# Kernel tuning notes

Measured on AMD Instinct MI355X. Metric: run time of the kernel, lower is better.

## Reference

```python
import jax, jax.numpy as jnp
import numpy as np
import math

N, S, D, H, L, F = 4, 2048, 512, 8, 4, 200
HD = D // H
EPS = 1e-5


def _pos_encoding(seq_len, d_model, dtype):
    pos = jnp.arange(seq_len, dtype=jnp.float32)[:, None]            # [S,1]
    div = jnp.exp(jnp.arange(0, d_model, 2, dtype=jnp.float32) * (-math.log(10000.0) / d_model))
    ang = pos * div                                                   # [S,D/2]
    pe = jnp.stack([jnp.sin(ang), jnp.cos(ang)], axis=-1).reshape(seq_len, d_model)
    return pe.astype(dtype)


def _layernorm(x, w, b):
    mu = jnp.mean(x, axis=-1, keepdims=True)
    var = jnp.mean(jnp.square(x - mu), axis=-1, keepdims=True)
    return (x - mu) * jax.lax.rsqrt(var + EPS) * w + b


def setup_inputs() -> dict:
    key = jax.random.key(0)
    ks = jax.random.split(key, 8)
    std = 0.02
    inp = {
        "features": jax.random.normal(ks[0], (N, S, D), dtype=jnp.float32),
        # attention projections, stored as [L, in, out] (math-equivalent to torch x @ W.T + b)
        "Wq": jax.random.normal(ks[1], (L, D, D), dtype=jnp.float32) * std,
        "bq": jnp.zeros((L, D), dtype=jnp.float32),
        "Wk": jax.random.normal(ks[2], (L, D, D), dtype=jnp.float32) * std,
        "bk": jnp.zeros((L, D), dtype=jnp.float32),
        "Wv": jax.random.normal(ks[3], (L, D, D), dtype=jnp.float32) * std,
        "bv": jnp.zeros((L, D), dtype=jnp.float32),
        "Wo": jax.random.normal(ks[4], (L, D, D), dtype=jnp.float32) * std,
        "bo": jnp.zeros((L, D), dtype=jnp.float32),
        # FFN
        "W1": jax.random.normal(ks[5], (L, D, F), dtype=jnp.float32) * std,
        "b1": jnp.zeros((L, F), dtype=jnp.float32),
        "W2": jax.random.normal(ks[6], (L, F, D), dtype=jnp.float32) * std,
        "b2": jnp.zeros((L, D), dtype=jnp.float32),
        # layernorms
        "ln1_w": jnp.ones((L, D), dtype=jnp.float32),
        "ln1_b": jnp.zeros((L, D), dtype=jnp.float32),
        "ln2_w": jnp.ones((L, D), dtype=jnp.float32),
        "ln2_b": jnp.zeros((L, D), dtype=jnp.float32),
    }
    return inp


def _encoder(features, Wq, bq, Wk, bk, Wv, bv, Wo, bo, W1, b1, W2, b2,
             ln1_w, ln1_b, ln2_w, ln2_b):
    n, s, d = features.shape
    x = features + _pos_encoding(s, d, features.dtype)[None]  # PositionalEncoding (dropout=identity in eval)
    scale = 1.0 / math.sqrt(HD)
    for l in range(L):
        # MultiHeadAttention: manual QK^T -> softmax -> AV
        q = (x @ Wq[l] + bq[l]).reshape(n, s, H, HD)
        k = (x @ Wk[l] + bk[l]).reshape(n, s, H, HD)
        v = (x @ Wv[l] + bv[l]).reshape(n, s, H, HD)
        attn = jnp.einsum("nshd,nthd->nhst", q, k) * scale          # [N,H,S,S]
        score = jax.nn.softmax(attn, axis=-1)
        y = jnp.einsum("nhst,nthd->nshd", score, v).reshape(n, s, d)
        attn_out = y @ Wo[l] + bo[l]
        x = _layernorm(x + attn_out, ln1_w[l], ln1_b[l])
        # FFN: linear2(relu(linear1(x)))
        ff = jax.nn.relu(x @ W1[l] + b1[l]) @ W2[l] + b2[l]
        x = _layernorm(x + ff, ln2_w[l], ln2_b[l])
    return x


def reference(features, Wq, bq, Wk, bk, Wv, bv, Wo, bo, W1, b1, W2, b2,
              ln1_w, ln1_b, ln2_w, ln2_b):
    return _encoder(features, Wq, bq, Wk, bk, Wv, bv, Wo, bo, W1, b1, W2, b2,
                    ln1_w, ln1_b, ln2_w, ln2_b)
```

## Files before the change

### kernel.cpp

```cpp
#include <hip/hip_runtime.h>
#include <hip/hip_bf16.h>
#include <cstdint>


typedef __bf16 bf16;
typedef __bf16 bf16x8 __attribute__((ext_vector_type(8)));
typedef __bf16 bf16x4 __attribute__((ext_vector_type(4)));
typedef float f32x4 __attribute__((ext_vector_type(4)));

#define MFMA16(a, b, c) __builtin_amdgcn_mfma_f32_16x16x32_bf16((a), (b), (c), 0, 0, 0)

static constexpr int NB   = 4;
static constexpr int SQ   = 2048;
static constexpr int DM   = 512;
static constexpr int NH   = 8;
static constexpr int HD   = 64;
static constexpr int NL   = 4;
static constexpr int FF   = 200;
static constexpr int FFP  = 256;
static constexpr int MTOK = NB * SQ;

__device__ __forceinline__ float fast_exp2(float x) {
#if __has_builtin(__builtin_amdgcn_exp2f)
    return __builtin_amdgcn_exp2f(x);
#else
    return exp2f(x);
#endif
}

__device__ __forceinline__ void gld16(bf16* l, const bf16* g) {
    __builtin_amdgcn_global_load_lds(
        (const __attribute__((address_space(1))) void*)g,
        (__attribute__((address_space(3))) void*)l, 16, 0, 0);
}

__device__ __forceinline__ void drain_and_barrier() {
    asm volatile("s_waitcnt vmcnt(0) lgkmcnt(0)" ::: "memory");
    __builtin_amdgcn_s_barrier();
}

__global__ __launch_bounds__(256) void convw_kernel(
    const float* __restrict__ Wq, const float* __restrict__ Wk,
    const float* __restrict__ Wv, const float* __restrict__ Wo,
    const float* __restrict__ W1, const float* __restrict__ W2,
    bf16* __restrict__ wqkvt, bf16* __restrict__ wot,
    bf16* __restrict__ w1t, bf16* __restrict__ w2t)
{
    __shared__ float tile[32][33];
    const int z = blockIdx.z, l = z / 6, which = z % 6;
    const float* src; bf16* dst; int K, Nsrc, Npad, Kpad;
    switch (which) {
        case 0: src = Wq + (size_t)l*DM*DM; dst = wqkvt + (size_t)(l*3+0)*DM*DM; K=DM; Nsrc=DM; Npad=DM; Kpad=DM; break;
        case 1: src = Wk + (size_t)l*DM*DM; dst = wqkvt + (size_t)(l*3+1)*DM*DM; K=DM; Nsrc=DM; Npad=DM; Kpad=DM; break;
        case 2: src = Wv + (size_t)l*DM*DM; dst = wqkvt + (size_t)(l*3+2)*DM*DM; K=DM; Nsrc=DM; Npad=DM; Kpad=DM; break;
        case 3: src = Wo + (size_t)l*DM*DM; dst = wot   + (size_t)l*DM*DM;       K=DM; Nsrc=DM; Npad=DM; Kpad=DM; break;
        case 4: src = W1 + (size_t)l*DM*FF; dst = w1t   + (size_t)l*FFP*DM;      K=DM; Nsrc=FF; Npad=FFP; Kpad=DM; break;
        default:src = W2 + (size_t)l*FF*DM; dst = w2t   + (size_t)l*DM*FFP;      K=FF; Nsrc=DM; Npad=DM; Kpad=FFP; break;
    }
    const int k0 = blockIdx.x * 32, n0 = blockIdx.y * 32;
    if (k0 >= Kpad || n0 >= Npad) return;
    const int tr = threadIdx.x >> 3, tc = (threadIdx.x & 7) * 4;
    for (int c = 0; c < 4; c++) {
        int sr = k0 + tr, sc = n0 + tc + c;
        tile[tr][tc + c] = (sr < K && sc < Nsrc) ? src[(size_t)sr * Nsrc + sc] : 0.f;
    }
    __syncthreads();
    const int dr = n0 + tr;
    if (dr < Npad) {
        for (int c = 0; c < 4; c++) {
            int dc = k0 + tc + c;
            if (dc < Kpad) dst[(size_t)dr * Kpad + dc] = (bf16)tile[tc + c][tr];
        }
    }
}

__global__ __launch_bounds__(256) void posenc_kernel(
    const float* __restrict__ f, float* __restrict__ x, bf16* __restrict__ xb)
{
    const int t = blockIdx.x * 256 + threadIdx.x;
    const int d2 = t & 255, row = t >> 8, s = row & (SQ - 1);
    const float kfac = -0.03597789207803197f;
    float dv = __expf((float)d2 * kfac);
    float ang = (float)s * dv;
    float pe0 = sinf(ang), pe1 = cosf(ang);
    const size_t base = (size_t)row * DM + d2 * 2;
    float2 fv = *(const float2*)(f + base);
    float o0 = fv.x + pe0, o1 = fv.y + pe1;
    *(float2*)(x + base) = make_float2(o0, o1);
    union { bf16 h[2]; unsigned int u; } pk;
    pk.h[0] = (bf16)o0; pk.h[1] = (bf16)o1;
    *(unsigned int*)(xb + base) = pk.u;
}

__device__ __forceinline__ void gemm128_core(
    const bf16* __restrict__ A, const bf16* __restrict__ Wt, int K,
    int m0, int n0, bf16* As, bf16* Bs, f32x4 (&acc)[4][4])
{
    const int tid = threadIdx.x;
    const int w = tid >> 6, lane = tid & 63;
    const int l15 = lane & 15, quad = lane >> 4;
    const int srow = w * 16 + (lane >> 2);
    const int scol = (lane & 3) * 8;
    const bf16* Ag = A  + (size_t)(m0 + srow) * K + scol;
    const bf16* Bg = Wt + (size_t)(n0 + srow) * K + scol;
    const int wm = (w >> 1) * 64, wn = (w & 1) * 64;

    auto stage = [&](int buf, int k0) {
        bf16* AsW = As + buf * 4096 + w * 512;
        bf16* BsW = Bs + buf * 4096 + w * 512;
        gld16(AsW,        Ag + k0);
        gld16(AsW + 2048, Ag + (size_t)64 * K + k0);
        gld16(BsW,        Bg + k0);
        gld16(BsW + 2048, Bg + (size_t)64 * K + k0);
    };

    stage(0, 0);
    drain_and_barrier();

    const int nsteps = K >> 5;
    int buf = 0;
    for (int t = 0; t < nsteps; ++t) {
        if (t + 1 < nsteps) stage(buf ^ 1, (t + 1) << 5);
        const bf16* AsR = As + buf * 4096;
        const bf16* BsR = Bs + buf * 4096;
        bf16x8 af[4], bfr[4];
        #pragma unroll
        for (int i = 0; i < 4; i++)
            af[i] = *(const bf16x8*)&AsR[(wm + i * 16 + l15) * 32 + quad * 8];
        #pragma unroll
        for (int j = 0; j < 4; j++)
            bfr[j] = *(const bf16x8*)&BsR[(wn + j * 16 + l15) * 32 + quad * 8];
        #pragma unroll
        for (int i = 0; i < 4; i++)
            #pragma unroll
            for (int j = 0; j < 4; j++)
                acc[i][j] = MFMA16(af[i], bfr[j], acc[i][j]);
        drain_and_barrier();
        buf ^= 1;
    }
}

__global__ __launch_bounds__(256, 4) void gemm64_kernel(
    const bf16* __restrict__ A, const bf16* __restrict__ Wt,
    const float* __restrict__ bias, int nbias,
    float* __restrict__ outf, bf16* __restrict__ outb,
    int K, int Nc, int mode)
{
    __shared__ alignas(16) bf16 As[2 * 128 * 32];
    __shared__ alignas(16) bf16 Bs[2 * 64 * 32];
    const int m0 = blockIdx.x * 128, n0 = blockIdx.y * 64;
    const int tid = threadIdx.x;
    const int w = tid >> 6, lane = tid & 63;
    const int l15 = lane & 15, quad = lane >> 4;
    const int srow = w * 16 + (lane >> 2);
    const int scol = (lane & 3) * 8;
    const bf16* Ag = A  + (size_t)(m0 + srow) * K + scol;
    const bf16* Bg = Wt + (size_t)(n0 + srow) * K + scol;
    const int wm = (w >> 1) * 64, wn = (w & 1) * 32;
    f32x4 acc[4][2] = {};

    auto stage = [&](int buf, int k0) {
        bf16* AsW = As + buf * 4096 + w * 512;
        bf16* BsW = Bs + buf * 2048 + w * 512;
        gld16(AsW,        Ag + k0);
        gld16(AsW + 2048, Ag + (size_t)64 * K + k0);
        gld16(BsW,        Bg + k0);
    };

    stage(0, 0);
    drain_and_barrier();

    const int nsteps = K >> 5;
    int buf = 0;
    for (int t = 0; t < nsteps; ++t) {
        if (t + 1 < nsteps) stage(buf ^ 1, (t + 1) << 5);
        const bf16* AsR = As + buf * 4096;
        const bf16* BsR = Bs + buf * 2048;
        bf16x8 af[4], bfr[2];
        #pragma unroll
        for (int i = 0; i < 4; i++)
            af[i] = *(const bf16x8*)&AsR[(wm + i * 16 + l15) * 32 + quad * 8];
        #pragma unroll
        for (int j = 0; j < 2; j++)
            bfr[j] = *(const bf16x8*)&BsR[(wn + j * 16 + l15) * 32 + quad * 8];
        #pragma unroll
        for (int i = 0; i < 4; i++)
            #pragma unroll
            for (int j = 0; j < 2; j++)
                acc[i][j] = MFMA16(af[i], bfr[j], acc[i][j]);
        drain_and_barrier();
        buf ^= 1;
    }

    #pragma unroll
    for (int j = 0; j < 2; j++) {
        const int col = n0 + wn + j * 16 + l15;
        const float bv = (col < nbias) ? bias[col] : 0.f;
        #pragma unroll
        for (int i = 0; i < 4; i++) {
            const int rbase = m0 + wm + i * 16 + quad * 4;
            #pragma unroll
            for (int r = 0; r < 4; r++) {
                float v = acc[i][j][r] + bv;
                const int row = rbase + r;
                const size_t idx = (size_t)row * Nc + col;
                if (mode == 0)      outf[idx] = v;
                else if (mode == 1) outb[idx] = (bf16)v;
                else                outb[idx] = (bf16)fmaxf(v, 0.f);
            }
        }
    }
}

__global__ __launch_bounds__(256, 4) void gemm_wo_kernel(
    const bf16* __restrict__ o0, const bf16* __restrict__ o1,
    const float* __restrict__ lpart,
    const bf16* __restrict__ Wt, const float* __restrict__ bias,
    float* __restrict__ outf)
{
    __shared__ alignas(16) bf16 As[2 * 128 * 32];
    __shared__ alignas(16) bf16 Bs[2 * 64 * 32];
    const int m0 = blockIdx.x * 128, n0 = blockIdx.y * 64;
    const int tid = threadIdx.x;
    const int w = tid >> 6, lane = tid & 63;
    const int l15 = lane & 15, quad = lane >> 4;
    const int srow = w * 16 + (lane >> 2);
    const int scol = (lane & 3) * 8;
    const int row0 = m0 + srow, row1 = row0 + 64;
    const bf16* Bg = Wt + (size_t)(n0 + srow) * DM + scol;
    const int wm = (w >> 1) * 64, wn = (w & 1) * 32;

    const int b0 = (((row0 >> 11) * 8) << 11) | (row0 & (SQ - 1));
    const int b1 = (((row1 >> 11) * 8) << 11) | (row1 & (SQ - 1));
    float rl0[8], rl1[8];
    #pragma unroll
    for (int h = 0; h < 8; h++) {
        rl0[h] = 1.f / (lpart[b0 + (h << 11)] + lpart[65536 + b0 + (h << 11)]);
        rl1[h] = 1.f / (lpart[b1 + (h << 11)] + lpart[65536 + b1 + (h << 11)]);
    }

    const bf16* A0g  = o0 + (size_t)row0 * DM + scol;
    const bf16* A0g2 = o0 + (size_t)row1 * DM + scol;
    const bf16* A1g  = o1 + (size_t)row0 * DM + scol;
    const bf16* A1g2 = o1 + (size_t)row1 * DM + scol;
    f32x4 acc[4][2] = {};

    auto combineStore = [&](int buf, int h, bf16x8 a0, bf16x8 c0, bf16x8 a1, bf16x8 c1) {
        bf16x8 s0, s1;
        #pragma unroll
        for (int i = 0; i < 8; i++) {
            s0[i] = (bf16)(((float)a0[i] + (float)c0[i]) * rl0[h]);
            s1[i] = (bf16)(((float)a1[i] + (float)c1[i]) * rl1[h]);
        }
        bf16* d = As + buf * 4096 + w * 512 + lane * 8;
        *(bf16x8*)d          = s0;
        *(bf16x8*)(d + 2048) = s1;
    };

    {
        bf16x8 a0 = *(const bf16x8*)(A0g);
        bf16x8 c0 = *(const bf16x8*)(A1g);
        bf16x8 a1 = *(const bf16x8*)(A0g2);
        bf16x8 c1 = *(const bf16x8*)(A1g2);
        gld16(Bs + w * 512, Bg);
        combineStore(0, 0, a0, c0, a1, c1);
        drain_and_barrier();
    }

    int buf = 0;
    for (int t = 0; t < 16; ++t) {
        const bool pre = (t + 1 < 16);
        bf16x8 na0, nc0, na1, nc1;
        if (pre) {
            const int k1 = (t + 1) * 32;
            na0 = *(const bf16x8*)(A0g  + k1);
            nc0 = *(const bf16x8*)(A1g  + k1);
            na1 = *(const bf16x8*)(A0g2 + k1);
            nc1 = *(const bf16x8*)(A1g2 + k1);
            gld16(Bs + (buf ^ 1) * 2048 + w * 512, Bg + k1);
        }

        const bf16* AsR = As + buf * 4096;
        const bf16* BsR = Bs + buf * 2048;
        bf16x8 af[4], bfr[2];
        #pragma unroll
        for (int i = 0; i < 4; i++)
            af[i] = *(const bf16x8*)&AsR[(wm + i * 16 + l15) * 32 + quad * 8];
        #pragma unroll
        for (int j = 0; j < 2; j++)
            bfr[j] = *(const bf16x8*)&BsR[(wn + j * 16 + l15) * 32 + quad * 8];
        #pragma unroll
        for (int i = 0; i < 4; i++)
            #pragma unroll
            for (int j = 0; j < 2; j++)
                acc[i][j] = MFMA16(af[i], bfr[j], acc[i][j]);

        if (pre) combineStore(buf ^ 1, (t + 1) >> 1, na0, nc0, na1, nc1);
        drain_and_barrier();
        buf ^= 1;
    }

    #pragma unroll
    for (int j = 0; j < 2; j++) {
        const int col = n0 + wn + j * 16 + l15;
        const float bv = bias[col];
        #pragma unroll
        for (int i = 0; i < 4; i++) {
            const int rbase = m0 + wm + i * 16 + quad * 4;
            #pragma unroll
            for (int r = 0; r < 4; r++)
                outf[(size_t)(rbase + r) * DM + col] = acc[i][j][r] + bv;
        }
    }
}

__global__ __launch_bounds__(256, 4) void gemm128_qkv_kernel(
    const bf16* __restrict__ xb, const bf16* __restrict__ Wt,
    const float* __restrict__ bq, const float* __restrict__ bk,
    const float* __restrict__ bv,
    bf16* __restrict__ qb, bf16* __restrict__ kb, bf16* __restrict__ vtb)
{
    __shared__ alignas(16) bf16 As[2 * 128 * 32];
    __shared__ alignas(16) bf16 Bs[2 * 128 * 32];
    const int m0 = blockIdx.x * 128, n0 = blockIdx.y * 128;
    f32x4 acc[4][4] = {};
    gemm128_core(xb, Wt, DM, m0, n0, As, Bs, acc);

    const int lane = threadIdx.x & 63;
    const int l15 = lane & 15, quad = lane >> 4;
    const int w = threadIdx.x >> 6;
    const int wm = (w >> 1) * 64, wn = (w & 1) * 64;
    const int which = n0 >> 9;
    const float* bias = (which == 0) ? bq : (which == 1) ? bk : bv;
    const float scale = (which == 0) ? 0.18033688f : 1.f;
    #pragma unroll
    for (int j = 0; j < 4; j++) {
        const int c = (n0 & 511) + wn + j * 16 + l15;
        const float bvv = bias[c];
        #pragma unroll
        for (int i = 0; i < 4; i++) {
            const int rbase = m0 + wm + i * 16 + quad * 4;
            if (which == 2) {
                union { bf16 h[4]; uint2 u2; } pk;
                #pragma unroll
                for (int r = 0; r < 4; r++)
                    pk.h[r] = (bf16)(acc[i][j][r] + bvv);
                const int n = rbase >> 11, s = rbase & (SQ - 1);
                const int h = c >> 6, hd = c & 63;
                *(uint2*)&vtb[((size_t)(((n << 3) | h) << 6 | hd) << 11) | s] = pk.u2;
            } else {
                #pragma unroll
                for (int r = 0; r < 4; r++) {
                    float v = (acc[i][j][r] + bvv) * scale;
                    const int row = rbase + r;
                    if (which == 0) qb[(size_t)row * DM + c] = (bf16)v;
                    else            kb[(size_t)row * DM + c] = (bf16)v;
                }
            }
        }
    }
}

__global__ __launch_bounds__(256, 2) void attn_kernel(
    const bf16* __restrict__ qb, const bf16* __restrict__ kb,
    const bf16* __restrict__ vtb,
    bf16* __restrict__ opart0, bf16* __restrict__ opart1,
    float* __restrict__ lpart)
{
    __shared__ alignas(16) bf16 Kt[2][64][72];
    __shared__ alignas(16) bf16 Vt[2 * 64 * 68];
    const int tid = threadIdx.x;
    const int w = tid >> 6, lane = tid & 63;
    const int l15 = lane & 15, quad = lane >> 4;
    const int id = blockIdx.x;
    const int kvhalf = id & 1;
    const int nh = (id >> 1) & 31;
    const int qblk = id >> 6;
    const int n = nh >> 3, h = nh & 7;
    const int q0 = qblk * 256 + w * 64;
    const int kvbase = kvhalf * (SQ / 2);
    const bf16* qbase = qb + (size_t)n * SQ * DM + h * HD;
    const bf16* kbase = kb + (size_t)n * SQ * DM + h * HD;
    const bf16* vbase = vtb + (size_t)nh * HD * SQ;

    bf16x8 qf[4][2];
    #pragma unroll
    for (int mi = 0; mi < 4; mi++)
        #pragma unroll
        for (int hh = 0; hh < 2; hh++)
            qf[mi][hh] = *(const bf16x8*)(qbase + (size_t)(q0 + mi*16 + l15) * DM + hh*32 + quad*8);

    bf16x8 ones8;
    #pragma unroll
    for (int i = 0; i < 8; i++) ones8[i] = (bf16)1.0f;

    f32x4 o[4][4] = {};
    f32x4 lacc[4] = {};

    const int srow = tid >> 2, seg = (tid & 3) * 16;
    const bf16* krow = kbase + (size_t)(kvbase + srow) * DM + seg;
    const bf16* vrow = vbase + (size_t)srow * SQ + kvbase + seg;

    auto storeV = [&](int buf, bf16x8 a, bf16x8 b) {
        bf16* d = &Vt[(buf * 64 + srow) * 68 + seg];
        bf16x4 p0, p1, p2, p3;
        #pragma unroll
        for (int i = 0; i < 4; i++) { p0[i]=a[i]; p1[i]=a[i+4]; p2[i]=b[i]; p3[i]=b[i+4]; }
        *(bf16x4*)(d)      = p0;
        *(bf16x4*)(d + 4)  = p1;
        *(bf16x4*)(d + 8)  = p2;
        *(bf16x4*)(d + 12) = p3;
    };

    {
        bf16x8 k0 = *(const bf16x8*)(krow);
        bf16x8 k1 = *(const bf16x8*)(krow + 8);
        bf16x8 v0 = *(const bf16x8*)(vrow);
        bf16x8 v1 = *(const bf16x8*)(vrow + 8);
        *(bf16x8*)&Kt[0][srow][seg]     = k0;
        *(bf16x8*)&Kt[0][srow][seg + 8] = k1;
        storeV(0, v0, v1);
    }

    const int NT = SQ / 128;
    for (int jt = 0; jt < NT; jt++) {
        const int buf = jt & 1;
        __syncthreads();
        const bool pre = (jt + 1 < NT);
        bf16x8 k0, k1, v0, v1;
        if (pre) {
            const bf16* kp = krow + (size_t)(jt + 1) * 64 * DM;
            const bf16* vp = vrow + (jt + 1) * 64;
            k0 = *(const bf16x8*)(kp);
            k1 = *(const bf16x8*)(kp + 8);
            v0 = *(const bf16x8*)(vp);
            v1 = *(const bf16x8*)(vp + 8);
        }

        #pragma unroll
        for (int sp = 0; sp < 2; sp++) {
            bf16x8 kfA0 = *(const bf16x8*)&Kt[buf][sp*32 + l15][quad*8];
            bf16x8 kfA1 = *(const bf16x8*)&Kt[buf][sp*32 + l15][32 + quad*8];
            bf16x8 kfB0 = *(const bf16x8*)&Kt[buf][sp*32 + 16 + l15][quad*8];
            bf16x8 kfB1 = *(const bf16x8*)&Kt[buf][sp*32 + 16 + l15][32 + quad*8];
            bf16x8 pf[4];
            #pragma unroll
            for (int mi = 0; mi < 4; mi++) {
                f32x4 sa = {}, sb = {};
                sa = MFMA16(kfA0, qf[mi][0], sa);
                sa = MFMA16(kfA1, qf[mi][1], sa);
                sb = MFMA16(kfB0, qf[mi][0], sb);
                sb = MFMA16(kfB1, qf[mi][1], sb);
                bf16x8 p;
                #pragma unroll
                for (int r = 0; r < 4; r++) {
                    p[r]     = (bf16)fast_exp2(sa[r]);
                    p[r + 4] = (bf16)fast_exp2(sb[r]);
                }
                pf[mi] = p;
                lacc[mi] = MFMA16(p, ones8, lacc[mi]);
            }
            #pragma unroll
            for (int d4 = 0; d4 < 4; d4++) {
                const bf16* vp2 = &Vt[(buf*64 + d4*16 + l15) * 68 + sp*32 + quad*4];
                bf16x4 vlo = *(const bf16x4*)(vp2);
                bf16x4 vhi = *(const bf16x4*)(vp2 + 16);
                bf16x8 vf;
                #pragma unroll
                for (int i = 0; i < 4; i++) { vf[i] = vlo[i]; vf[i+4] = vhi[i]; }
                #pragma unroll
                for (int mi = 0; mi < 4; mi++)
                    o[mi][d4] = MFMA16(pf[mi], vf, o[mi][d4]);
            }
        }

        if (pre) {
            *(bf16x8*)&Kt[buf^1][srow][seg]     = k0;
            *(bf16x8*)&Kt[buf^1][srow][seg + 8] = k1;
            storeV(buf^1, v0, v1);
        }
    }

    if (l15 == 0) {
        const int base = (kvhalf << 16) + (nh << 11) + q0 + quad * 4;
        #pragma unroll
        for (int mi = 0; mi < 4; mi++) {
            float4 v4 = make_float4(lacc[mi][0], lacc[mi][1], lacc[mi][2], lacc[mi][3]);
            *(float4*)&lpart[base + mi * 16] = v4;
        }
    }

    bf16* op = kvhalf ? opart1 : opart0;
    #pragma unroll
    for (int mi = 0; mi < 4; mi++) {
        #pragma unroll
        for (int d4 = 0; d4 < 4; d4++) {
            const int col = h * HD + d4 * 16 + l15;
            #pragma unroll
            for (int r = 0; r < 4; r++) {
                const int row = n * SQ + q0 + mi*16 + quad*4 + r;
                op[(size_t)row * DM + col] = (bf16)o[mi][d4][r];
            }
        }
    }
}

__global__ __launch_bounds__(256) void ln_kernel(
    const float* __restrict__ res, const float* __restrict__ add,
    const float* __restrict__ g, const float* __restrict__ beta,
    float* __restrict__ outf, bf16* __restrict__ outb)
{
    const int w = threadIdx.x >> 6, lane = threadIdx.x & 63;
    const size_t row = (size_t)blockIdx.x * 4 + w;
    const float4* rp = (const float4*)(res + row * DM);
    const float4* ap = (const float4*)(add + row * DM);
    float4 v[2];
    float s = 0.f, s2 = 0.f;
    #pragma unroll
    for (int i = 0; i < 2; i++) {
        const int idx = i * 64 + lane;
        float4 a = rp[idx], c = ap[idx];
        float x0 = a.x + c.x, x1 = a.y + c.y, x2 = a.z + c.z, x3 = a.w + c.w;
        v[i] = make_float4(x0, x1, x2, x3);
        s  += x0 + x1 + x2 + x3;
        s2 += x0*x0 + x1*x1 + x2*x2 + x3*x3;
    }
    for (int m = 1; m < 64; m <<= 1) {
        s  += __shfl_xor(s,  m, 64);
        s2 += __shfl_xor(s2, m, 64);
    }
    const float mean = s * (1.f / DM);
    const float var  = s2 * (1.f / DM) - mean * mean;
    const float rstd = rsqrtf(var + 1e-5f);
    #pragma unroll
    for (int i = 0; i < 2; i++) {
        const int idx = i * 64 + lane;
        float4 gw = ((const float4*)g)[idx], bw = ((const float4*)beta)[idx];
        float o0 = (v[i].x - mean) * rstd * gw.x + bw.x;
        float o1 = (v[i].y - mean) * rstd * gw.y + bw.y;
        float o2 = (v[i].z - mean) * rstd * gw.z + bw.z;
        float o3 = (v[i].w - mean) * rstd * gw.w + bw.w;
        ((float4*)(outf + row * DM))[idx] = make_float4(o0, o1, o2, o3);
        union { bf16 h[4]; uint2 u; } pk;
        pk.h[0] = (bf16)o0; pk.h[1] = (bf16)o1; pk.h[2] = (bf16)o2; pk.h[3] = (bf16)o3;
        *(uint2*)(outb + row * DM + idx * 4) = pk.u;
    }
}

extern "C" void kernel_launch(void* const* d_in, const int* in_sizes, int n_in,
                              void* d_out, int out_size, void* d_ws, size_t ws_size,
                              hipStream_t stream)
{
    const float* features = (const float*)d_in[0];
    const float* Wq  = (const float*)d_in[1];
    const float* bq  = (const float*)d_in[2];
    const float* Wk  = (const float*)d_in[3];
    const float* bk  = (const float*)d_in[4];
    const float* Wv  = (const float*)d_in[5];
    const float* bv  = (const float*)d_in[6];
    const float* Wo  = (const float*)d_in[7];
    const float* bo  = (const float*)d_in[8];
    const float* W1  = (const float*)d_in[9];
    const float* b1  = (const float*)d_in[10];
    const float* W2  = (const float*)d_in[11];
    const float* b2  = (const float*)d_in[12];
    const float* ln1w = (const float*)d_in[13];
    const float* ln1b = (const float*)d_in[14];
    const float* ln2w = (const float*)d_in[15];
    const float* ln2b = (const float*)d_in[16];
    float* outp = (float*)d_out;

    char* p = (char*)d_ws;
    size_t off = 0;
    auto alloc = [&](size_t bytes) { void* r = p + off; off = (off + bytes + 255) & ~(size_t)255; return r; };
    const size_t tokD = (size_t)MTOK * DM;
    float* x     = (float*)alloc(tokD * 4);
    float* tmp   = (float*)alloc(tokD * 4);
    bf16* xb     = (bf16*)alloc(tokD * 2);
    bf16* qb     = (bf16*)alloc(tokD * 2);
    bf16* kb     = (bf16*)alloc(tokD * 2);
    bf16* vtb    = (bf16*)alloc(tokD * 2);
    bf16* opart0 = (bf16*)alloc(tokD * 2);
    bf16* opart1 = (bf16*)alloc(tokD * 2);
    float* lpart = (float*)alloc(2 * 65536 * 4);
    bf16* ffh    = (bf16*)alloc((size_t)MTOK * FFP * 2);
    bf16* wqkvt  = (bf16*)alloc((size_t)NL * 3 * DM * DM * 2);
    bf16* wot    = (bf16*)alloc((size_t)NL * DM * DM * 2);
    bf16* w1t    = (bf16*)alloc((size_t)NL * FFP * DM * 2);
    bf16* w2t    = (bf16*)alloc((size_t)NL * DM * FFP * 2);
    (void)ws_size; (void)in_sizes; (void)n_in; (void)out_size;

    convw_kernel<<<dim3(16, 16, NL * 6), 256, 0, stream>>>(
        Wq, Wk, Wv, Wo, W1, W2, wqkvt, wot, w1t, w2t);

    posenc_kernel<<<MTOK, 256, 0, stream>>>(features, x, xb);

    for (int l = 0; l < NL; l++) {
        const bf16* wqkvt_l = wqkvt + (size_t)l * 3 * DM * DM;
        gemm128_qkv_kernel<<<dim3(MTOK / 128, 1536 / 128), 256, 0, stream>>>(
            xb, wqkvt_l, bq + l*DM, bk + l*DM, bv + l*DM, qb, kb, vtb);
        attn_kernel<<<512, 256, 0, stream>>>(qb, kb, vtb, opart0, opart1, lpart);
        gemm_wo_kernel<<<dim3(MTOK / 128, DM / 64), 256, 0, stream>>>(
            opart0, opart1, lpart, wot + (size_t)l*DM*DM, bo + l*DM, tmp);
        ln_kernel<<<MTOK / 4, 256, 0, stream>>>(x, tmp, ln1w + l*DM, ln1b + l*DM, x, xb);
        gemm64_kernel<<<dim3(MTOK / 128, FFP / 64), 256, 0, stream>>>(
            xb, w1t + (size_t)l*FFP*DM, b1 + l*FF, FF, nullptr, ffh, DM, FFP, 2);
        gemm64_kernel<<<dim3(MTOK / 128, DM / 64), 256, 0, stream>>>(
            ffh, w2t + (size_t)l*DM*FFP, b2 + l*DM, DM, tmp, nullptr, FFP, DM, 0);
        float* outdst = (l == NL - 1) ? outp : x;
        ln_kernel<<<MTOK / 4, 256, 0, stream>>>(x, tmp, ln2w + l*DM, ln2b + l*DM, outdst, xb);
    }
}
```

Before: 604.9 us.

## Triple-buffer GEMM shared-memory staging with partial vmcnt waits

Converts the double-buffered LDS staging in the 128x128 and 128x64 GEMM cores to a three-slot ring. Two tiles are prefetched, and each iteration waits only for the oldest outstanding loads via s_waitcnt vmcnt(N). A single barrier per step replaces the full drain-and-barrier, so global loads for later tiles overlap with MFMA work. LDS usage grows by half and QKV launch bounds drop to 3 blocks/SM, which may reduce occupancy. Correctness depends on the vmcnt count matching the number of loads issued per stage.

After: 602.6 us. About the same (-0.4%).

```diff
diff --git a/kernel.cpp b/kernel.cpp
--- a/kernel.cpp
+++ b/kernel.cpp
@@ -114,13 +114,21 @@
         gld16(BsW + 2048, Bg + (size_t)64 * K + k0);
     };
 
+    const int nsteps = K >> 5;
     stage(0, 0);
-    drain_and_barrier();
-
-    const int nsteps = K >> 5;
+    stage(1, 32);
+
     int buf = 0;
     for (int t = 0; t < nsteps; ++t) {
-        if (t + 1 < nsteps) stage(buf ^ 1, (t + 1) << 5);
+        if (t + 1 < nsteps)
+            asm volatile("s_waitcnt vmcnt(4)" ::: "memory");
+        else
+            asm volatile("s_waitcnt vmcnt(0)" ::: "memory");
+        __builtin_amdgcn_s_barrier();
+        if (t + 2 < nsteps) {
+            int b2 = buf + 2; if (b2 >= 3) b2 -= 3;
+            stage(b2, (t + 2) << 5);
+        }
         const bf16* AsR = As + buf * 4096;
         const bf16* BsR = Bs + buf * 4096;
         bf16x8 af[4], bfr[4];
@@ -135,8 +143,7 @@
             #pragma unroll
             for (int j = 0; j < 4; j++)
                 acc[i][j] = MFMA16(af[i], bfr[j], acc[i][j]);
-        drain_and_barrier();
-        buf ^= 1;
+        buf = (buf == 2) ? 0 : buf + 1;
     }
 }
 
@@ -146,8 +153,8 @@
     float* __restrict__ outf, bf16* __restrict__ outb,
     int K, int Nc, int mode)
 {
-    __shared__ alignas(16) bf16 As[2 * 128 * 32];
-    __shared__ alignas(16) bf16 Bs[2 * 64 * 32];
+    __shared__ alignas(16) bf16 As[3 * 128 * 32];
+    __shared__ alignas(16) bf16 Bs[3 * 64 * 32];
     const int m0 = blockIdx.x * 128, n0 = blockIdx.y * 64;
     const int tid = threadIdx.x;
     const int w = tid >> 6, lane = tid & 63;
@@ -167,13 +174,21 @@
         gld16(BsW,        Bg + k0);
     };
 
+    const int nsteps = K >> 5;
     stage(0, 0);
-    drain_and_barrier();
-
-    const int nsteps = K >> 5;
+    stage(1, 32);
+
     int buf = 0;
     for (int t = 0; t < nsteps; ++t) {
-        if (t + 1 < nsteps) stage(buf ^ 1, (t + 1) << 5);
+        if (t + 1 < nsteps)
+            asm volatile("s_waitcnt vmcnt(3)" ::: "memory");
+        else
+            asm volatile("s_waitcnt vmcnt(0)" ::: "memory");
+        __builtin_amdgcn_s_barrier();
+        if (t + 2 < nsteps) {
+            int b2 = buf + 2; if (b2 >= 3) b2 -= 3;
+            stage(b2, (t + 2) << 5);
+        }
         const bf16* AsR = As + buf * 4096;
         const bf16* BsR = Bs + buf * 2048;
         bf16x8 af[4], bfr[2];
@@ -188,8 +203,7 @@
             #pragma unroll
             for (int j = 0; j < 2; j++)
                 acc[i][j] = MFMA16(af[i], bfr[j], acc[i][j]);
-        drain_and_barrier();
-        buf ^= 1;
+        buf = (buf == 2) ? 0 : buf + 1;
     }
 
     #pragma unroll
@@ -314,14 +328,14 @@
     }
 }
 
-__global__ __launch_bounds__(256, 4) void gemm128_qkv_kernel(
+__global__ __launch_bounds__(256, 3) void gemm128_qkv_kernel(
     const bf16* __restrict__ xb, const bf16* __restrict__ Wt,
     const float* __restrict__ bq, const float* __restrict__ bk,
     const float* __restrict__ bv,
     bf16* __restrict__ qb, bf16* __restrict__ kb, bf16* __restrict__ vtb)
 {
-    __shared__ alignas(16) bf16 As[2 * 128 * 32];
-    __shared__ alignas(16) bf16 Bs[2 * 128 * 32];
+    __shared__ alignas(16) bf16 As[3 * 128 * 32];
+    __shared__ alignas(16) bf16 Bs[3 * 128 * 32];
     const int m0 = blockIdx.x * 128, n0 = blockIdx.y * 128;
     f32x4 acc[4][4] = {};
     gemm128_core(xb, Wt, DM, m0, n0, As, Bs, acc);
```
